# Optimization experiments

Hardware: AMD Instinct MI355X
Metric: run time of the kernel (lower is better)

## Reference

```python
import jax, jax.numpy as jnp
import numpy as np

B, S, D, H = 4, 2048, 1024, 16
DH = D // H


def setup_inputs() -> dict:
    key = jax.random.key(0)
    k0, k1, k2, k3 = jax.random.split(key, 4)
    x = jax.random.normal(k0, (B, S, D), dtype=jnp.float32)
    k = jax.random.normal(k1, (B, H, S, DH), dtype=jnp.float32)
    v = jax.random.normal(k2, (B, H, S, DH), dtype=jnp.float32)
    # nn.Linear(d, d, bias=False) weight: [out, in]; scaled like torch default init
    Wq = jax.random.normal(k3, (D, D), dtype=jnp.float32) * (1.0 / np.sqrt(D))
    return {"x": x, "k": k, "v": v, "Wq": Wq}


def reference(x, k, v, Wq):
    Bx, Sx, d = x.shape
    h, dh = k.shape[1], k.shape[3]
    rd = jnp.sqrt(jnp.float32(d))  # NOTE: module scales by sqrt(d), not sqrt(d_head)
    # q projection: y = x @ Wq.T  -> [B,S,d] -> [B,h,S,dh]
    q = (x @ Wq.T).reshape(Bx, Sx, h, dh).transpose(0, 2, 1, 3)
    # scores [B,h,S,S]
    a = jnp.einsum('bhqd,bhkd->bhqk', q, k) / rd
    causal = jnp.triu(jnp.ones((Sx, Sx), dtype=bool), k=1)
    a = jnp.where(causal, -jnp.inf, a)
    p = jax.nn.softmax(a, axis=-1)
    o = jnp.einsum('bhqk,bhkd->bhqd', p, v)  # [B,h,S,dh]
    o = o.transpose(0, 2, 1, 3).reshape(Bx, Sx, d)
    return x + o
```

## Files before the change

### kernel.cpp

```cpp
#include <hip/hip_runtime.h>
#include <hip/hip_bf16.h>

typedef __attribute__((ext_vector_type(4))) float f32x4;
typedef __attribute__((ext_vector_type(8))) short bf16x8;
typedef __attribute__((ext_vector_type(4))) unsigned short u16x4;

#define MFMA16(a, b, c) __builtin_amdgcn_mfma_f32_16x16x32_bf16((a), (b), (c), 0, 0, 0)

static __device__ __forceinline__ unsigned short f2bf(float f) {
    unsigned u = __float_as_uint(f);
    u += 0x7FFFu + ((u >> 16) & 1u);
    return (unsigned short)(u >> 16);
}
static __device__ __forceinline__ uint2 pack4_rhu(float4 v) {
    unsigned a = __float_as_uint(v.x) + 0x8000u;
    unsigned b = __float_as_uint(v.y) + 0x8000u;
    unsigned c = __float_as_uint(v.z) + 0x8000u;
    unsigned d = __float_as_uint(v.w) + 0x8000u;
    uint2 r;
    r.x = __builtin_amdgcn_perm(b, a, 0x07060302u);
    r.y = __builtin_amdgcn_perm(d, c, 0x07060302u);
    return r;
}
static __device__ __forceinline__ float exp2_fast(float x) {
#if __has_builtin(__builtin_amdgcn_exp2f)
    return __builtin_amdgcn_exp2f(x);
#else
    return exp2f(x);
#endif
}

#define QSCALE 0.04508422002778011f

__global__ __launch_bounds__(256) void prep_kernel(const float* __restrict__ x,
                                                   const float* __restrict__ wq,
                                                   const float* __restrict__ vin,
                                                   unsigned short* __restrict__ qout,
                                                   unsigned short* __restrict__ vt) {
    __shared__ __align__(16) unsigned short As[2][128][40];
    __shared__ __align__(16) unsigned short Bs[2][128][40];
    const int bid = blockIdx.x;
    const int tid = threadIdx.x;

    if (bid < 512) {
        const int m0 = (bid & 63) * 128;
        const int n0 = (bid >> 6) * 128;
        const int wave = tid >> 6, lane = tid & 63;
        const int lg = lane >> 4, lc = lane & 15;
        const int wm = wave >> 1, wn = wave & 1;

        f32x4 acc[4][4];
#pragma unroll
        for (int i = 0; i < 4; ++i)
#pragma unroll
            for (int j = 0; j < 4; ++j) acc[i][j] = (f32x4){0.f, 0.f, 0.f, 0.f};

        float4 ax[4], bx[4];
#pragma unroll
        for (int i = 0; i < 4; ++i) {
            int c = tid + i * 256;
            int row = c >> 3, kc = (c & 7) * 4;
            ax[i] = *(const float4*)(x  + (size_t)(m0 + row) * 1024 + kc);
            bx[i] = *(const float4*)(wq + (size_t)(n0 + row) * 1024 + kc);
        }
#pragma unroll
        for (int i = 0; i < 4; ++i) {
            int c = tid + i * 256;
            int row = c >> 3, kc = (c & 7) * 4;
            *(uint2*)&As[0][row][kc] = pack4_rhu(ax[i]);
            *(uint2*)&Bs[0][row][kc] = pack4_rhu(bx[i]);
        }

        int cur = 0;
        for (int ki = 0; ki < 32; ++ki) {
            __syncthreads();
            const bool havenext = (ki + 1 < 32);
            if (havenext) {
                int ks = (ki + 1) * 32;
#pragma unroll
                for (int i = 0; i < 4; ++i) {
                    int c = tid + i * 256;
                    int row = c >> 3, kc = (c & 7) * 4;
                    ax[i] = *(const float4*)(x  + (size_t)(m0 + row) * 1024 + ks + kc);
                    bx[i] = *(const float4*)(wq + (size_t)(n0 + row) * 1024 + ks + kc);
                }
            }
            bf16x8 af[4], bfr[4];
#pragma unroll
            for (int i = 0; i < 4; ++i) {
                af[i]  = *(const bf16x8*)&As[cur][wm * 64 + i * 16 + lc][lg * 8];
                bfr[i] = *(const bf16x8*)&Bs[cur][wn * 64 + i * 16 + lc][lg * 8];
            }
            __builtin_amdgcn_s_setprio(1);
#pragma unroll
            for (int mi = 0; mi < 4; ++mi)
#pragma unroll
                for (int ni = 0; ni < 4; ++ni)
                    acc[mi][ni] = MFMA16(af[mi], bfr[ni], acc[mi][ni]);
            __builtin_amdgcn_s_setprio(0);
            if (havenext) {
#pragma unroll
                for (int i = 0; i < 4; ++i) {
                    int c = tid + i * 256;
                    int row = c >> 3, kc = (c & 7) * 4;
                    *(uint2*)&As[cur ^ 1][row][kc] = pack4_rhu(ax[i]);
                    *(uint2*)&Bs[cur ^ 1][row][kc] = pack4_rhu(bx[i]);
                }
            }
            cur ^= 1;
        }
#pragma unroll
        for (int mi = 0; mi < 4; ++mi)
#pragma unroll
            for (int ni = 0; ni < 4; ++ni)
#pragma unroll
                for (int r = 0; r < 4; ++r) {
                    int m = m0 + wm * 64 + mi * 16 + lg * 4 + r;
                    int n = n0 + wn * 64 + ni * 16 + lc;
                    int b = m >> 11, s = m & 2047;
                    int h = n >> 6, dh = n & 63;
                    qout[(((size_t)b * 16 + h) * 2048 + s) * 64 + dh] = f2bf(acc[mi][ni][r] * QSCALE);
                }
    } else {
        float (*buf)[65] = (float (*)[65])(&As[0][0][0]);
        const int idx = bid - 512;
        const int s0 = (idx & 31) * 64;
        const int bh = idx >> 5;
#pragma unroll
        for (int i = 0; i < 4; ++i) {
            int c = tid + i * 256;
            int s = c >> 4, dc = (c & 15) * 4;
            float4 val = *(const float4*)(vin + ((size_t)bh * 2048 + s0 + s) * 64 + dc);
            buf[s][dc] = val.x; buf[s][dc + 1] = val.y; buf[s][dc + 2] = val.z; buf[s][dc + 3] = val.w;
        }
        __syncthreads();
#pragma unroll
        for (int i = 0; i < 4; ++i) {
            int c = tid + i * 256;
            int dh = c >> 4, sc = (c & 15) * 4;
            u16x4 o = { f2bf(buf[sc][dh]), f2bf(buf[sc + 1][dh]), f2bf(buf[sc + 2][dh]), f2bf(buf[sc + 3][dh]) };
            *(u16x4*)(vt + ((size_t)bh * 64 + dh) * 2048 + s0 + sc) = o;
        }
    }
}

__global__ __launch_bounds__(256, 3) void attn_kernel(const unsigned short* __restrict__ qg,
                                                      const float* __restrict__ kg32,
                                                      const unsigned short* __restrict__ vtg,
                                                      const float* __restrict__ x,
                                                      float* __restrict__ outp) {
    __shared__ __align__(16) unsigned short Ks[2][64][64];
    __shared__ __align__(16) unsigned short VTs[2][64][64];
    __shared__ __align__(16) unsigned short Ps[4][32][76];

    const int bh = blockIdx.x;
    const int qb = 15 - blockIdx.y;
    const int b = bh >> 4, h = bh & 15;
    const int tid = threadIdx.x;
    const int wave = tid >> 6, lane = tid & 63;
    const int lg = lane >> 4, lc = lane & 15;
    const int lc7 = lc & 7;
    const int qw0 = qb * 128 + wave * 32;
    const int nkv = 2 * qb + 2;

    const int r0  = tid >> 3;
    const int c16 = tid & 7;
    const int swz = (c16 ^ (r0 & 7)) * 8;
    const float* kbase = kg32 + ((size_t)bh * 2048 + r0) * 64 + c16 * 8;
    const unsigned short* vbase = vtg + ((size_t)bh * 64 + r0) * 2048 + c16 * 8;

    bf16x8 qf[2][2];
#pragma unroll
    for (int qt = 0; qt < 2; ++qt)
#pragma unroll
        for (int c = 0; c < 2; ++c)
            qf[qt][c] = *(const bf16x8*)(qg + ((size_t)bh * 2048 + qw0 + qt * 16 + lc) * 64 + c * 32 + lg * 8);

    f32x4 oacc[2][4];
#pragma unroll
    for (int qt = 0; qt < 2; ++qt)
#pragma unroll
        for (int dt = 0; dt < 4; ++dt) oacc[qt][dt] = (f32x4){0.f, 0.f, 0.f, 0.f};
    float l_r[2] = {0.f, 0.f};

    {
        union { uint2 u[2]; bf16x8 v; } cka, ckb;
        cka.u[0] = pack4_rhu(*(const float4*)(kbase));
        cka.u[1] = pack4_rhu(*(const float4*)(kbase + 4));
        ckb.u[0] = pack4_rhu(*(const float4*)(kbase + 2048));
        ckb.u[1] = pack4_rhu(*(const float4*)(kbase + 2052));
        *(bf16x8*)&Ks[0][r0][swz]       = cka.v;
        *(bf16x8*)&Ks[0][r0 + 32][swz]  = ckb.v;
        *(bf16x8*)&VTs[0][r0][swz]      = *(const bf16x8*)(vbase);
        *(bf16x8*)&VTs[0][r0 + 32][swz] = *(const bf16x8*)(vbase + 65536);
    }

    int cur = 0;
    for (int kv = 0; kv < nkv; ++kv) {
        __syncthreads();

        const bool havenext = (kv + 1 < nkv);
        const int nxt = havenext ? kv + 1 : kv;
        float4 nka0 = *(const float4*)(kbase + (size_t)nxt * 4096);
        float4 nka1 = *(const float4*)(kbase + (size_t)nxt * 4096 + 4);
        float4 nkb0 = *(const float4*)(kbase + (size_t)nxt * 4096 + 2048);
        float4 nkb1 = *(const float4*)(kbase + (size_t)nxt * 4096 + 2052);
        bf16x8 nv0 = *(const bf16x8*)(vbase + nxt * 64);
        bf16x8 nv1 = *(const bf16x8*)(vbase + nxt * 64 + 65536);

        const bool active = (kv * 64 <= qw0 + 31);
        if (active) {
            bf16x8 kf[4][2];
#pragma unroll
            for (int kt = 0; kt < 4; ++kt)
#pragma unroll
                for (int c = 0; c < 2; ++c)
                    kf[kt][c] = *(const bf16x8*)&Ks[cur][kt * 16 + lc][((4 * c + lg) ^ lc7) * 8];

            const int kvb = kv * 64;
#pragma unroll
            for (int qt = 0; qt < 2; ++qt) {
                f32x4 st[4];
                __builtin_amdgcn_s_setprio(1);
#pragma unroll
                for (int kt = 0; kt < 4; ++kt) {
                    f32x4 a = (f32x4){0.f, 0.f, 0.f, 0.f};
                    a = MFMA16(kf[kt][0], qf[qt][0], a);
                    a = MFMA16(kf[kt][1], qf[qt][1], a);
                    st[kt] = a;
                }
                __builtin_amdgcn_s_setprio(0);

                float pp[4][4];
#pragma unroll
                for (int kt = 0; kt < 4; ++kt)
#pragma unroll
                    for (int r = 0; r < 4; ++r) pp[kt][r] = st[kt][r];
                if (kvb + 63 > qw0 + qt * 16) {
                    const int qrow = qw0 + qt * 16 + lc;
#pragma unroll
                    for (int kt = 0; kt < 4; ++kt)
#pragma unroll
                        for (int r = 0; r < 4; ++r) {
                            int kk = kvb + kt * 16 + lg * 4 + r;
                            if (kk > qrow) pp[kt][r] = -1e30f;
                        }
                }
                float rs = 0.f;
#pragma unroll
                for (int kt = 0; kt < 4; ++kt)
#pragma unroll
                    for (int r = 0; r < 4; ++r) {
                        float e = exp2_fast(pp[kt][r]);
                        pp[kt][r] = e;
                        rs += e;
                    }
                l_r[qt] += rs;
#pragma unroll
                for (int kt = 0; kt < 4; ++kt) {
                    uint2 w;
                    w.x = __builtin_amdgcn_perm(__float_as_uint(pp[kt][1]), __float_as_uint(pp[kt][0]), 0x07060302u);
                    w.y = __builtin_amdgcn_perm(__float_as_uint(pp[kt][3]), __float_as_uint(pp[kt][2]), 0x07060302u);
                    *(uint2*)&Ps[wave][qt * 16 + lc][kt * 16 + lg * 4] = w;
                }
            }
            asm volatile("s_waitcnt lgkmcnt(0)" ::: "memory");

            bf16x8 pf[2][2];
#pragma unroll
            for (int qt = 0; qt < 2; ++qt)
#pragma unroll
                for (int c = 0; c < 2; ++c)
                    pf[qt][c] = *(const bf16x8*)&Ps[wave][qt * 16 + lc][c * 32 + lg * 8];
            __builtin_amdgcn_s_setprio(1);
#pragma unroll
            for (int dt = 0; dt < 4; ++dt)
#pragma unroll
                for (int c = 0; c < 2; ++c) {
                    bf16x8 vtf = *(const bf16x8*)&VTs[cur][dt * 16 + lc][((4 * c + lg) ^ lc7) * 8];
#pragma unroll
                    for (int qt = 0; qt < 2; ++qt)
                        oacc[qt][dt] = MFMA16(vtf, pf[qt][c], oacc[qt][dt]);
                }
            __builtin_amdgcn_s_setprio(0);
        }

        if (havenext) {
            union { uint2 u[2]; bf16x8 v; } cka, ckb;
            cka.u[0] = pack4_rhu(nka0);
            cka.u[1] = pack4_rhu(nka1);
            ckb.u[0] = pack4_rhu(nkb0);
            ckb.u[1] = pack4_rhu(nkb1);
            *(bf16x8*)&Ks[cur ^ 1][r0][swz]       = cka.v;
            *(bf16x8*)&Ks[cur ^ 1][r0 + 32][swz]  = ckb.v;
            *(bf16x8*)&VTs[cur ^ 1][r0][swz]      = nv0;
            *(bf16x8*)&VTs[cur ^ 1][r0 + 32][swz] = nv1;
        }
        cur ^= 1;
    }

#pragma unroll
    for (int qt = 0; qt < 2; ++qt) {
        float lt = l_r[qt];
        lt += __shfl_xor(lt, 16, 64);
        lt += __shfl_xor(lt, 32, 64);
        float li = 1.0f / lt;
        const int q = qw0 + qt * 16 + lc;
        const size_t obase = ((size_t)b * 2048 + q) * 1024 + (size_t)h * 64 + lg * 4;
#pragma unroll
        for (int dt = 0; dt < 4; ++dt) {
            const size_t oi = obase + dt * 16;
            float4 xv = *(const float4*)(x + oi);
            float4 ov;
            ov.x = xv.x + oacc[qt][dt][0] * li;
            ov.y = xv.y + oacc[qt][dt][1] * li;
            ov.z = xv.z + oacc[qt][dt][2] * li;
            ov.w = xv.w + oacc[qt][dt][3] * li;
            *(float4*)(outp + oi) = ov;
        }
    }
}

extern "C" void kernel_launch(void* const* d_in, const int* in_sizes, int n_in,
                              void* d_out, int out_size, void* d_ws, size_t ws_size,
                              hipStream_t stream) {
    const float* x  = (const float*)d_in[0];
    const float* k  = (const float*)d_in[1];
    const float* v  = (const float*)d_in[2];
    const float* wq = (const float*)d_in[3];
    float* outp = (float*)d_out;

    const size_t NELEM = (size_t)4 * 2048 * 1024;
    unsigned short* qbuf  = (unsigned short*)d_ws;
    unsigned short* vtbuf = qbuf + NELEM;

    prep_kernel<<<512 + 2048, 256, 0, stream>>>(x, wq, v, qbuf, vtbuf);
    attn_kernel<<<dim3(64, 16), 256, 0, stream>>>(qbuf, k, vtbuf, x, outp);
}
```

Before: 91.82 us.

## Split long causal query blocks across two workgroups with ticket-based merge

Query blocks 8-15 now have their KV range split in half across two workgroups, scheduled from a table that balances work. The grid grows from 16 to 24 rows. Each half writes its partial output (as bf16) and row sums to a workspace, and the last half to arrive, detected with an atomic ticket, merges both and writes the final output. K/V tiles become single-buffered with an extra barrier, the launch-bounds occupancy hint is dropped, and the P tile gets an XOR swizzle. The aim is to cut the tail caused by long causal rows, in exchange for extra global traffic, a memset, atomics and less load/compute overlap.

```diff
diff --git a/kernel.cpp b/kernel.cpp
--- a/kernel.cpp
+++ b/kernel.cpp
@@ -22,6 +22,9 @@
     r.y = __builtin_amdgcn_perm(d, c, 0x07060302u);
     return r;
 }
+static __device__ __forceinline__ float bf2f(unsigned v) {
+    return __uint_as_float(v << 16);
+}
 static __device__ __forceinline__ float exp2_fast(float x) {
 #if __has_builtin(__builtin_amdgcn_exp2f)
     return __builtin_amdgcn_exp2f(x);
@@ -144,24 +147,36 @@
     }
 }
 
-__global__ __launch_bounds__(256, 3) void attn_kernel(const unsigned short* __restrict__ qg,
-                                                      const float* __restrict__ kg32,
-                                                      const unsigned short* __restrict__ vtg,
-                                                      const float* __restrict__ x,
-                                                      float* __restrict__ outp) {
-    __shared__ __align__(16) unsigned short Ks[2][64][64];
-    __shared__ __align__(16) unsigned short VTs[2][64][64];
-    __shared__ __align__(16) unsigned short Ps[4][32][76];
+__global__ __launch_bounds__(256) void attn_kernel(const unsigned short* __restrict__ qg,
+                                                   const float* __restrict__ kg32,
+                                                   const unsigned short* __restrict__ vtg,
+                                                   const float* __restrict__ x,
+                                                   float* __restrict__ outp,
+                                                   unsigned short* __restrict__ Opart,
+                                                   float* __restrict__ lpart,
+                                                   unsigned int* __restrict__ tickets) {
+    __shared__ __align__(16) unsigned short Ks[64][64];
+    __shared__ __align__(16) unsigned short VTs[64][64];
+    __shared__ __align__(16) unsigned short Ps[4][32][64];
+
+    static const unsigned char tab[24] = {
+        62, 63, 28, 58, 59, 54, 55, 24, 50, 51, 46, 47,
+        20, 42, 43, 38, 39, 16, 34, 35, 12, 8, 4, 0
+    };
+    const unsigned code = tab[blockIdx.y];
+    const int qb = code >> 2;
+    const int split = (code >> 1) & 1;
+    const int half = code & 1;
+    const int kv0 = (split && half) ? (qb + 1) : 0;
+    const int kv1 = split ? (half ? (2 * qb + 2) : (qb + 1)) : (2 * qb + 2);
 
     const int bh = blockIdx.x;
-    const int qb = 15 - blockIdx.y;
     const int b = bh >> 4, h = bh & 15;
     const int tid = threadIdx.x;
     const int wave = tid >> 6, lane = tid & 63;
     const int lg = lane >> 4, lc = lane & 15;
     const int lc7 = lc & 7;
     const int qw0 = qb * 128 + wave * 32;
-    const int nkv = 2 * qb + 2;
 
     const int r0  = tid >> 3;
     const int c16 = tid & 7;
@@ -185,21 +200,20 @@
 
     {
         union { uint2 u[2]; bf16x8 v; } cka, ckb;
-        cka.u[0] = pack4_rhu(*(const float4*)(kbase));
-        cka.u[1] = pack4_rhu(*(const float4*)(kbase + 4));
-        ckb.u[0] = pack4_rhu(*(const float4*)(kbase + 2048));
-        ckb.u[1] = pack4_rhu(*(const float4*)(kbase + 2052));
-        *(bf16x8*)&Ks[0][r0][swz]       = cka.v;
-        *(bf16x8*)&Ks[0][r0 + 32][swz]  = ckb.v;
-        *(bf16x8*)&VTs[0][r0][swz]      = *(const bf16x8*)(vbase);
-        *(bf16x8*)&VTs[0][r0 + 32][swz] = *(const bf16x8*)(vbase + 65536);
+        cka.u[0] = pack4_rhu(*(const float4*)(kbase + (size_t)kv0 * 4096));
+        cka.u[1] = pack4_rhu(*(const float4*)(kbase + (size_t)kv0 * 4096 + 4));
+        ckb.u[0] = pack4_rhu(*(const float4*)(kbase + (size_t)kv0 * 4096 + 2048));
+        ckb.u[1] = pack4_rhu(*(const float4*)(kbase + (size_t)kv0 * 4096 + 2052));
+        *(bf16x8*)&Ks[r0][swz]       = cka.v;
+        *(bf16x8*)&Ks[r0 + 32][swz]  = ckb.v;
+        *(bf16x8*)&VTs[r0][swz]      = *(const bf16x8*)(vbase + kv0 * 64);
+        *(bf16x8*)&VTs[r0 + 32][swz] = *(const bf16x8*)(vbase + kv0 * 64 + 65536);
     }
 
-    int cur = 0;
-    for (int kv = 0; kv < nkv; ++kv) {
+    for (int kv = kv0; kv < kv1; ++kv) {
         __syncthreads();
 
-        const bool havenext = (kv + 1 < nkv);
+        const bool havenext = (kv + 1 < kv1);
         const int nxt = havenext ? kv + 1 : kv;
         float4 nka0 = *(const float4*)(kbase + (size_t)nxt * 4096);
         float4 nka1 = *(const float4*)(kbase + (size_t)nxt * 4096 + 4);
@@ -215,7 +229,7 @@
             for (int kt = 0; kt < 4; ++kt)
 #pragma unroll
                 for (int c = 0; c < 2; ++c)
-                    kf[kt][c] = *(const bf16x8*)&Ks[cur][kt * 16 + lc][((4 * c + lg) ^ lc7) * 8];
+                    kf[kt][c] = *(const bf16x8*)&Ks[kt * 16 + lc][((4 * c + lg) ^ lc7) * 8];
 
             const int kvb = kv * 64;
 #pragma unroll
@@ -261,7 +275,7 @@
                     uint2 w;
                     w.x = __builtin_amdgcn_perm(__float_as_uint(pp[kt][1]), __float_as_uint(pp[kt][0]), 0x07060302u);
                     w.y = __builtin_amdgcn_perm(__float_as_uint(pp[kt][3]), __float_as_uint(pp[kt][2]), 0x07060302u);
-                    *(uint2*)&Ps[wave][qt * 16 + lc][kt * 16 + lg * 4] = w;
+                    *(uint2*)&Ps[wave][qt * 16 + lc][((kt * 2 + (lg >> 1)) ^ lc7) * 8 + (lg & 1) * 4] = w;
                 }
             }
             asm volatile("s_waitcnt lgkmcnt(0)" ::: "memory");
@@ -271,13 +285,13 @@
             for (int qt = 0; qt < 2; ++qt)
 #pragma unroll
                 for (int c = 0; c < 2; ++c)
-                    pf[qt][c] = *(const bf16x8*)&Ps[wave][qt * 16 + lc][c * 32 + lg * 8];
+                    pf[qt][c] = *(const bf16x8*)&Ps[wave][qt * 16 + lc][((c * 4 + lg) ^ lc7) * 8];
             __builtin_amdgcn_s_setprio(1);
 #pragma unroll
             for (int dt = 0; dt < 4; ++dt)
 #pragma unroll
                 for (int c = 0; c < 2; ++c) {
-                    bf16x8 vtf = *(const bf16x8*)&VTs[cur][dt * 16 + lc][((4 * c + lg) ^ lc7) * 8];
+                    bf16x8 vtf = *(const bf16x8*)&VTs[dt * 16 + lc][((4 * c + lg) ^ lc7) * 8];
 #pragma unroll
                     for (int qt = 0; qt < 2; ++qt)
                         oacc[qt][dt] = MFMA16(vtf, pf[qt][c], oacc[qt][dt]);
@@ -285,38 +299,103 @@
             __builtin_amdgcn_s_setprio(0);
         }
 
+        __syncthreads();
         if (havenext) {
             union { uint2 u[2]; bf16x8 v; } cka, ckb;
             cka.u[0] = pack4_rhu(nka0);
             cka.u[1] = pack4_rhu(nka1);
             ckb.u[0] = pack4_rhu(nkb0);
             ckb.u[1] = pack4_rhu(nkb1);
-            *(bf16x8*)&Ks[cur ^ 1][r0][swz]       = cka.v;
-            *(bf16x8*)&Ks[cur ^ 1][r0 + 32][swz]  = ckb.v;
-            *(bf16x8*)&VTs[cur ^ 1][r0][swz]      = nv0;
-            *(bf16x8*)&VTs[cur ^ 1][r0 + 32][swz] = nv1;
-        }
-        cur ^= 1;
+            *(bf16x8*)&Ks[r0][swz]       = cka.v;
+            *(bf16x8*)&Ks[r0 + 32][swz]  = ckb.v;
+            *(bf16x8*)&VTs[r0][swz]      = nv0;
+            *(bf16x8*)&VTs[r0 + 32][swz] = nv1;
+        }
     }
 
+    float lt[2];
 #pragma unroll
     for (int qt = 0; qt < 2; ++qt) {
-        float lt = l_r[qt];
-        lt += __shfl_xor(lt, 16, 64);
-        lt += __shfl_xor(lt, 32, 64);
-        float li = 1.0f / lt;
-        const int q = qw0 + qt * 16 + lc;
-        const size_t obase = ((size_t)b * 2048 + q) * 1024 + (size_t)h * 64 + lg * 4;
-#pragma unroll
-        for (int dt = 0; dt < 4; ++dt) {
-            const size_t oi = obase + dt * 16;
-            float4 xv = *(const float4*)(x + oi);
-            float4 ov;
-            ov.x = xv.x + oacc[qt][dt][0] * li;
-            ov.y = xv.y + oacc[qt][dt][1] * li;
-            ov.z = xv.z + oacc[qt][dt][2] * li;
-            ov.w = xv.w + oacc[qt][dt][3] * li;
-            *(float4*)(outp + oi) = ov;
+        float t = l_r[qt];
+        t += __shfl_xor(t, 16, 64);
+        t += __shfl_xor(t, 32, 64);
+        lt[qt] = t;
+    }
+
+    if (!split) {
+#pragma unroll
+        for (int qt = 0; qt < 2; ++qt) {
+            float li = 1.0f / lt[qt];
+            const int q = qw0 + qt * 16 + lc;
+            const size_t obase = ((size_t)b * 2048 + q) * 1024 + (size_t)h * 64 + lg * 4;
+#pragma unroll
+            for (int dt = 0; dt < 4; ++dt) {
+                const size_t oi = obase + dt * 16;
+                float4 xv = *(const float4*)(x + oi);
+                float4 ov;
+                ov.x = xv.x + oacc[qt][dt][0] * li;
+                ov.y = xv.y + oacc[qt][dt][1] * li;
+                ov.z = xv.z + oacc[qt][dt][2] * li;
+                ov.w = xv.w + oacc[qt][dt][3] * li;
+                *(float4*)(outp + oi) = ov;
+            }
+        }
+    } else {
+        const int p = bh * 8 + (qb - 8);
+        uint2 wk[2][4];
+#pragma unroll
+        for (int qt = 0; qt < 2; ++qt)
+#pragma unroll
+            for (int dt = 0; dt < 4; ++dt) {
+                float4 v = make_float4(oacc[qt][dt][0], oacc[qt][dt][1], oacc[qt][dt][2], oacc[qt][dt][3]);
+                wk[qt][dt] = pack4_rhu(v);
+            }
+        unsigned short* slot = Opart + ((size_t)(half * 512 + p)) * 8192 + tid * 32;
+#pragma unroll
+        for (int qt = 0; qt < 2; ++qt)
+#pragma unroll
+            for (int dt = 0; dt < 4; ++dt)
+                *(uint2*)(slot + (qt * 4 + dt) * 4) = wk[qt][dt];
+        float* lsl = lpart + ((size_t)(half * 512 + p)) * 512 + tid * 2;
+        lsl[0] = lt[0];
+        lsl[1] = lt[1];
+        __syncthreads();
+        int* flagp = (int*)&Ps[0][0][0];
+        if (tid == 0) {
+            __threadfence();
+            unsigned old = atomicAdd(&tickets[p], 1u);
+            *flagp = (int)old;
+        }
+        __syncthreads();
+        if (*flagp == 0) return;
+        __threadfence();
+        const unsigned short* pslot = Opart + ((size_t)((1 - half) * 512 + p)) * 8192 + tid * 32;
+        const float* plsl = lpart + ((size_t)((1 - half) * 512 + p)) * 512 + tid * 2;
+        float li[2];
+        li[0] = 1.0f / (lt[0] + plsl[0]);
+        li[1] = 1.0f / (lt[1] + plsl[1]);
+#pragma unroll
+        for (int qt = 0; qt < 2; ++qt) {
+            const int q = qw0 + qt * 16 + lc;
+            const size_t obase = ((size_t)b * 2048 + q) * 1024 + (size_t)h * 64 + lg * 4;
+#pragma unroll
+            for (int dt = 0; dt < 4; ++dt) {
+                uint2 pw = *(const uint2*)(pslot + (qt * 4 + dt) * 4);
+                uint2 ow = wk[qt][dt];
+                float4 f;
+                f.x = bf2f(ow.x & 0xffffu) + bf2f(pw.x & 0xffffu);
+                f.y = bf2f(ow.x >> 16)     + bf2f(pw.x >> 16);
+                f.z = bf2f(ow.y & 0xffffu) + bf2f(pw.y & 0xffffu);
+                f.w = bf2f(ow.y >> 16)     + bf2f(pw.y >> 16);
+                const size_t oi = obase + dt * 16;
+                float4 xv = *(const float4*)(x + oi);
+                float4 ov;
+                ov.x = xv.x + f.x * li[qt];
+                ov.y = xv.y + f.y * li[qt];
+                ov.z = xv.z + f.z * li[qt];
+                ov.w = xv.w + f.w * li[qt];
+                *(float4*)(outp + oi) = ov;
+            }
         }
     }
 }
@@ -333,7 +412,12 @@
     const size_t NELEM = (size_t)4 * 2048 * 1024;
     unsigned short* qbuf  = (unsigned short*)d_ws;
     unsigned short* vtbuf = qbuf + NELEM;
-
+    unsigned short* Opart = vtbuf + NELEM;
+    float* lpart = (float*)(Opart + (size_t)2 * 512 * 8192);
+    unsigned int* tickets = (unsigned int*)(lpart + (size_t)2 * 512 * 512);
+
+    hipMemsetAsync(tickets, 0, 512 * sizeof(unsigned int), stream);
     prep_kernel<<<512 + 2048, 256, 0, stream>>>(x, wq, v, qbuf, vtbuf);
-    attn_kernel<<<dim3(64, 16), 256, 0, stream>>>(qbuf, k, vtbuf, x, outp);
-}
+    attn_kernel<<<dim3(64, 24), 256, 0, stream>>>(qbuf, k, vtbuf, x, outp,
+                                                  Opart, lpart, tickets);
+}
```

After: 224.7 us. 145% more time.
